# Optimization experiments

Measured on AMD Instinct MI355X. Metric: run time of the kernel, lower is better.

Reference implementation:

```python
import jax, jax.numpy as jnp
import numpy as np

B, F, N, L, K = 16, 256, 16384, 4096, 9  # batch, channels, input pixels, pooled pixels, kernel


def setup_inputs() -> dict:
    key = jax.random.key(0)
    k1, k2 = jax.random.split(key, 2)
    input_images = jax.random.normal(k1, (B, F, N), dtype=jnp.float32)
    # raw indices in [-1, N-1]; -1 marks a missing neighbor (zero padding)
    raw = jax.random.randint(k2, (L, K), 0, N + 1) - 1
    mask = (raw != -1).astype(jnp.float32)          # prepare_mask: mask out -1 entries
    indices = jnp.maximum(raw, 0)                   # prepare_mask: clamp -1 -> 0
    return {"input_images": input_images, "indices": indices, "mask": mask}


def reference(input_images, indices, mask):
    # gather neighbor features: (B, F, L, K)
    col = input_images[..., indices] * mask
    # max over kernel (neighbor) axis -> pooled image (B, F, L)
    return jnp.max(col, axis=-1)
```

## Files before the change

kernel.cpp:

```cpp
#include <hip/hip_runtime.h>

#define B_ 16
#define F_ 256
#define N_ 16384
#define L_ 4096
#define K_ 9

#define NTHR 1024
#define NBLK 256
#define ROWS_PER_BLK (B_ * F_ / NBLK)

typedef const __attribute__((address_space(1))) void* gas_ptr;
typedef __attribute__((address_space(3))) void* las_ptr;

__global__ __launch_bounds__(256) void prep_comb_kernel(
    const int* __restrict__ idx, const float* __restrict__ mask,
    unsigned short* __restrict__ comb) {
  int t = blockIdx.x * blockDim.x + threadIdx.x;
  if (t >= L_ * K_) return;
  int l = t / K_;
  int k = t - l * K_;
  comb[k * L_ + l] =
      (mask[t] != 0.0f) ? (unsigned short)idx[t] : (unsigned short)N_;
}

__global__ __launch_bounds__(NTHR) void pool_pipe_kernel(
    const float* __restrict__ img, const unsigned short* __restrict__ comb,
    float* __restrict__ out) {
  __shared__ __align__(16) float buf[2][N_ + 16];
  const int tid = threadIdx.x;
  const int bid = blockIdx.x;
  const int lane = tid & 63;
  const int wv = tid >> 6;

  unsigned cpk[18];
#pragma unroll
  for (int j = 0; j < 18; ++j) {
    const int s0 = 2 * j, s1 = 2 * j + 1;
    const int it0 = s0 / K_, k0 = s0 % K_;
    const int it1 = s1 / K_, k1 = s1 % K_;
    unsigned a = comb[k0 * L_ + it0 * NTHR + tid];
    unsigned b = comb[k1 * L_ + it1 * NTHR + tid];
    cpk[j] = a | (b << 16);
  }

#define STAGE_ROW(row_, dstbuf_)                                              \
  {                                                                           \
    const float* src_ = img + (size_t)(row_)*N_;                              \
    _Pragma("unroll") for (int i_ = 0; i_ < 4; ++i_) {                        \
      const int c_ = i_ * 16 + wv;                                            \
      __builtin_amdgcn_global_load_lds((gas_ptr)(src_ + c_ * 256 + lane * 4), \
                                       (las_ptr)((dstbuf_) + c_ * 256),       \
                                       16, 0, 0);                             \
    }                                                                         \
  }

  STAGE_ROW(bid, &buf[0][0]);
  if (tid < 2) buf[tid][N_] = 0.0f;
  __syncthreads();

#pragma unroll 1
  for (int p = 0; p < ROWS_PER_BLK; ++p) {
    if (p + 1 < ROWS_PER_BLK) {
      STAGE_ROW((p + 1) * NBLK + bid, &buf[(p + 1) & 1][0]);
    }

    const float* row = &buf[p & 1][0];
    float* outp = out + (size_t)((size_t)p * NBLK + bid) * L_;
#pragma unroll
    for (int it = 0; it < L_ / NTHR; ++it) {
      int l = it * NTHR + tid;
      float v[K_];
#pragma unroll
      for (int k = 0; k < K_; ++k) {
        const int slot = it * K_ + k;
        unsigned w = cpk[slot >> 1];
        unsigned id = (slot & 1) ? (w >> 16) : (w & 0xffffu);
        v[k] = row[id];
      }
      float t0 = fmaxf(fmaxf(v[0], v[1]), v[2]);
      float t1 = fmaxf(fmaxf(v[3], v[4]), v[5]);
      float t2 = fmaxf(fmaxf(v[6], v[7]), v[8]);
      outp[l] = fmaxf(fmaxf(t0, t1), t2);
    }

    __syncthreads();
  }
#undef STAGE_ROW
}

__global__ __launch_bounds__(256) void pool_kernel_direct(
    const float* __restrict__ img, const int* __restrict__ idx,
    const float* __restrict__ mask, float* __restrict__ out) {
  __shared__ __align__(16) float row[N_ + 4];
  const int bf = blockIdx.x;
  const int tid = threadIdx.x;

  const float4* src4 = (const float4*)(img + (size_t)bf * N_);
  float4* row4 = (float4*)row;
#pragma unroll
  for (int i = 0; i < 16; ++i) {
    int j = i * 256 + tid;
    row4[j] = src4[j];
  }
  __syncthreads();

  float* outp = out + (size_t)bf * L_;
  for (int it = 0; it < L_ / 256; ++it) {
    int l = it * 256 + tid;
    float m = -INFINITY;
#pragma unroll
    for (int k = 0; k < K_; ++k) {
      int t = l * K_ + k;
      float v = (mask[t] != 0.0f) ? row[idx[t]] : 0.0f;
      m = fmaxf(m, v);
    }
    outp[l] = m;
  }
}

extern "C" void kernel_launch(void* const* d_in, const int* in_sizes, int n_in,
                              void* d_out, int out_size, void* d_ws, size_t ws_size,
                              hipStream_t stream) {
  const float* img = (const float*)d_in[0];
  const int* idx = (const int*)d_in[1];
  const float* mask = (const float*)d_in[2];
  float* out = (float*)d_out;

  const size_t comb_bytes = (size_t)L_ * K_ * sizeof(unsigned short);
  if (ws_size >= comb_bytes) {
    unsigned short* comb = (unsigned short*)d_ws;
    int total = L_ * K_;
    prep_comb_kernel<<<(total + 255) / 256, 256, 0, stream>>>(idx, mask, comb);
    pool_pipe_kernel<<<NBLK, NTHR, 0, stream>>>(img, comb, out);
  } else {
    pool_kernel_direct<<<B_ * F_, 256, 0, stream>>>(img, idx, mask, out);
  }
}
```

Before: 72.91 us.

## Fuse index prep into pooling kernel and relax end-of-iteration barrier

```diff
diff --git a/kernel.cpp b/kernel.cpp
--- a/kernel.cpp
+++ b/kernel.cpp
@@ -13,36 +13,14 @@
 typedef const __attribute__((address_space(1))) void* gas_ptr;
 typedef __attribute__((address_space(3))) void* las_ptr;
 
-__global__ __launch_bounds__(256) void prep_comb_kernel(
-    const int* __restrict__ idx, const float* __restrict__ mask,
-    unsigned short* __restrict__ comb) {
-  int t = blockIdx.x * blockDim.x + threadIdx.x;
-  if (t >= L_ * K_) return;
-  int l = t / K_;
-  int k = t - l * K_;
-  comb[k * L_ + l] =
-      (mask[t] != 0.0f) ? (unsigned short)idx[t] : (unsigned short)N_;
-}
-
-__global__ __launch_bounds__(NTHR) void pool_pipe_kernel(
-    const float* __restrict__ img, const unsigned short* __restrict__ comb,
-    float* __restrict__ out) {
+__global__ __launch_bounds__(NTHR) void pool_fused_kernel(
+    const float* __restrict__ img, const int* __restrict__ idx,
+    const float* __restrict__ mask, float* __restrict__ out) {
   __shared__ __align__(16) float buf[2][N_ + 16];
   const int tid = threadIdx.x;
   const int bid = blockIdx.x;
   const int lane = tid & 63;
   const int wv = tid >> 6;
-
-  unsigned cpk[18];
-#pragma unroll
-  for (int j = 0; j < 18; ++j) {
-    const int s0 = 2 * j, s1 = 2 * j + 1;
-    const int it0 = s0 / K_, k0 = s0 % K_;
-    const int it1 = s1 / K_, k1 = s1 % K_;
-    unsigned a = comb[k0 * L_ + it0 * NTHR + tid];
-    unsigned b = comb[k1 * L_ + it1 * NTHR + tid];
-    cpk[j] = a | (b << 16);
-  }
 
 #define STAGE_ROW(row_, dstbuf_)                                              \
   {                                                                           \
@@ -53,6 +31,17 @@
                                        (las_ptr)((dstbuf_) + c_ * 256),       \
                                        16, 0, 0);                             \
     }                                                                         \
+  }
+
+  unsigned cpk[18];
+#pragma unroll
+  for (int j = 0; j < 18; ++j) {
+    const int s0 = 2 * j, s1 = 2 * j + 1;
+    const int t0 = (s0 / K_ * NTHR + tid) * K_ + s0 % K_;
+    const int t1 = (s1 / K_ * NTHR + tid) * K_ + s1 % K_;
+    unsigned a = (mask[t0] != 0.0f) ? (unsigned)idx[t0] : (unsigned)N_;
+    unsigned b = (mask[t1] != 0.0f) ? (unsigned)idx[t1] : (unsigned)N_;
+    cpk[j] = a | (b << 16);
   }
 
   STAGE_ROW(bid, &buf[0][0]);
@@ -84,39 +73,12 @@
       outp[l] = fmaxf(fmaxf(t0, t1), t2);
     }
 
-    __syncthreads();
+    if (p + 1 < ROWS_PER_BLK) {
+      asm volatile("s_waitcnt vmcnt(4)" ::: "memory");
+      __builtin_amdgcn_s_barrier();
+    }
   }
 #undef STAGE_ROW
-}
-
-__global__ __launch_bounds__(256) void pool_kernel_direct(
-    const float* __restrict__ img, const int* __restrict__ idx,
-    const float* __restrict__ mask, float* __restrict__ out) {
-  __shared__ __align__(16) float row[N_ + 4];
-  const int bf = blockIdx.x;
-  const int tid = threadIdx.x;
-
-  const float4* src4 = (const float4*)(img + (size_t)bf * N_);
-  float4* row4 = (float4*)row;
-#pragma unroll
-  for (int i = 0; i < 16; ++i) {
-    int j = i * 256 + tid;
-    row4[j] = src4[j];
-  }
-  __syncthreads();
-
-  float* outp = out + (size_t)bf * L_;
-  for (int it = 0; it < L_ / 256; ++it) {
-    int l = it * 256 + tid;
-    float m = -INFINITY;
-#pragma unroll
-    for (int k = 0; k < K_; ++k) {
-      int t = l * K_ + k;
-      float v = (mask[t] != 0.0f) ? row[idx[t]] : 0.0f;
-      m = fmaxf(m, v);
-    }
-    outp[l] = m;
-  }
 }
 
 extern "C" void kernel_launch(void* const* d_in, const int* in_sizes, int n_in,
@@ -126,14 +88,5 @@
   const int* idx = (const int*)d_in[1];
   const float* mask = (const float*)d_in[2];
   float* out = (float*)d_out;
-
-  const size_t comb_bytes = (size_t)L_ * K_ * sizeof(unsigned short);
-  if (ws_size >= comb_bytes) {
-    unsigned short* comb = (unsigned short*)d_ws;
-    int total = L_ * K_;
-    prep_comb_kernel<<<(total + 255) / 256, 256, 0, stream>>>(idx, mask, comb);
-    pool_pipe_kernel<<<NBLK, NTHR, 0, stream>>>(img, comb, out);
-  } else {
-    pool_kernel_direct<<<B_ * F_, 256, 0, stream>>>(img, idx, mask, out);
-  }
+  pool_fused_kernel<<<NBLK, NTHR, 0, stream>>>(img, idx, mask, out);
 }
```

New measurement: 87.39 us. +19.9%, slower.
